# Performance work log

Measured on AMD Instinct MI355X. Metric: run time of the kernel, lower is better.

The kernel has to match this reference:

```python
import jax, jax.numpy as jnp
import numpy as np

IN_DIM = 1024
CTX_DIM = 768
NUM_HEADS = 16
HEAD_DIM = IN_DIM // NUM_HEADS
SCALE = 1.0 / float(np.sqrt(HEAD_DIM))


def setup_inputs() -> dict:
    key = jax.random.key(0)
    ks = jax.random.split(key, 10)
    B, NQ, NKV = 8, 1024, 512
    s_in = 1.0 / float(np.sqrt(IN_DIM))
    s_ctx = 1.0 / float(np.sqrt(CTX_DIM))
    return {
        "x": jax.random.normal(ks[0], (B, NQ, IN_DIM), dtype=jnp.float32),
        "context": jax.random.normal(ks[1], (B, NKV, CTX_DIM), dtype=jnp.float32),
        "Wq": jax.random.normal(ks[2], (IN_DIM, IN_DIM), dtype=jnp.float32) * s_in,
        "bq": jax.random.normal(ks[3], (IN_DIM,), dtype=jnp.float32) * 0.01,
        "Wk": jax.random.normal(ks[4], (IN_DIM, CTX_DIM), dtype=jnp.float32) * s_ctx,
        "bk": jax.random.normal(ks[5], (IN_DIM,), dtype=jnp.float32) * 0.01,
        "Wv": jax.random.normal(ks[6], (IN_DIM, CTX_DIM), dtype=jnp.float32) * s_ctx,
        "bv": jax.random.normal(ks[7], (IN_DIM,), dtype=jnp.float32) * 0.01,
        "Wo": jax.random.normal(ks[8], (IN_DIM, IN_DIM), dtype=jnp.float32) * s_in,
        "bo": jax.random.normal(ks[9], (IN_DIM,), dtype=jnp.float32) * 0.01,
    }


def reference(x, context, Wq, bq, Wk, bk, Wv, bv, Wo, bo):
    # Linear projections (torch Linear: y = x @ W.T + b)
    q = x @ Wq.T + bq              # [B, Nq, in_dim]
    k = context @ Wk.T + bk        # [B, Nkv, in_dim]
    v = context @ Wv.T + bv        # [B, Nkv, in_dim]
    B, NQ, _ = q.shape
    NKV = k.shape[1]
    q = q.reshape(B, NQ, NUM_HEADS, HEAD_DIM)
    k = k.reshape(B, NKV, NUM_HEADS, HEAD_DIM)
    v = v.reshape(B, NKV, NUM_HEADS, HEAD_DIM)
    attn = jnp.einsum('bihd,bjhd->bhij', q, k) * SCALE   # [B, H, Nq, Nkv]
    # the half-batch split in the original is mathematically identical to
    # a plain softmax over the last dim
    attn = jax.nn.softmax(attn, axis=-1)
    out = jnp.einsum('bhij,bjhd->bihd', attn, v)          # [B, Nq, H, Dh]
    out = out.reshape(B, NQ, IN_DIM)
    return out @ Wo.T + bo
```

## Files before the change

kernel.cpp:

```cpp
#include <hip/hip_runtime.h>
#include <math.h>

#define IN_DIM    1024
#define CTX_DIM   768
#define NUM_HEADS 16
#define HEAD_DIM  64
#define BATCH     8
#define NQ        1024
#define NKV       512
#define SCALE     0.125f

typedef __attribute__((ext_vector_type(8))) _Float16 f16x8;
typedef __attribute__((ext_vector_type(4))) _Float16 f16x4;
typedef __attribute__((ext_vector_type(4))) float    f32x4;

__device__ __forceinline__ void async16(const void* g, void* l) {
    __builtin_amdgcn_global_load_lds(
        (const __attribute__((address_space(1))) void*)g,
        (__attribute__((address_space(3))) void*)l, 16, 0, 0);
}

__global__ __launch_bounds__(256)
void cvt6(const float* __restrict__ s0, const float* __restrict__ s1,
          const float* __restrict__ s2, const float* __restrict__ s3,
          const float* __restrict__ s4, const float* __restrict__ s5,
          _Float16* __restrict__ dst)
{
    const int stride = gridDim.x * blockDim.x;
    for (int i = blockIdx.x * blockDim.x + threadIdx.x; i < 3801088; i += stride) {
        const float* s; int loc;
        if      (i < 2097152) { s = s0; loc = i; }
        else if (i < 2883584) { s = s1; loc = i - 2097152; }
        else if (i < 3145728) { s = s2; loc = i - 2883584; }
        else if (i < 3342336) { s = s3; loc = i - 3145728; }
        else if (i < 3538944) { s = s4; loc = i - 3342336; }
        else                  { s = s5; loc = i - 3538944; }
        float4 v = *(const float4*)(s + (size_t)loc * 4);
        f16x4 o;
        o.x = (_Float16)v.x; o.y = (_Float16)v.y;
        o.z = (_Float16)v.z; o.w = (_Float16)v.w;
        *(f16x4*)(dst + (size_t)i * 4) = o;
    }
}

template<int BN, typename OutT>
__global__ __launch_bounds__(256)
void gemm_h(const _Float16* __restrict__ A, const _Float16* __restrict__ W,
            const float* __restrict__ bias, OutT* __restrict__ C,
            int M, int N, int K)
{
    constexpr int BM = 128, BK = 64;
    constexpr int NF = BN / 32;
    __shared__ alignas(16) _Float16 As[BM * BK];
    __shared__ alignas(16) _Float16 Ws[BN * BK];

    const int tid = threadIdx.x;
    const int l   = tid & 63;
    const int w   = tid >> 6;
    const int wr  = w >> 1, wc = w & 1;
    const int m0  = blockIdx.y * BM;
    const int n0  = blockIdx.x * BN;

    f32x4 acc[4][NF];
    #pragma unroll
    for (int m = 0; m < 4; ++m)
        #pragma unroll
        for (int n = 0; n < NF; ++n)
            acc[m][n] = (f32x4){0.f, 0.f, 0.f, 0.f};

    const int nk = K / BK;
    for (int kt = 0; kt < nk; ++kt) {
        const int k0 = kt * BK;
        #pragma unroll
        for (int it = 0; it < 4; ++it) {
            int e = it * 256 + tid;
            int r = e >> 3, p = e & 7;
            async16(A + (size_t)(m0 + r) * K + k0 + ((p ^ (r & 7)) * 8),
                    &As[(size_t)(it * 256 + (tid & ~63)) * 8]);
        }
        #pragma unroll
        for (int it = 0; it < BN / 32; ++it) {
            int e = it * 256 + tid;
            int r = e >> 3, p = e & 7;
            async16(W + (size_t)(n0 + r) * K + k0 + ((p ^ (r & 7)) * 8),
                    &Ws[(size_t)(it * 256 + (tid & ~63)) * 8]);
        }
        __syncthreads();

        #pragma unroll
        for (int kk = 0; kk < 2; ++kk) {
            f16x8 af[4], bf[NF];
            #pragma unroll
            for (int m = 0; m < 4; ++m) {
                int rr = wr * 64 + m * 16 + (l & 15);
                int slot = (kk * 4 + (l >> 4)) ^ (rr & 7);
                af[m] = *(const f16x8*)&As[rr * 64 + slot * 8];
            }
            #pragma unroll
            for (int n = 0; n < NF; ++n) {
                int rr = wc * (BN / 2) + n * 16 + (l & 15);
                int slot = (kk * 4 + (l >> 4)) ^ (rr & 7);
                bf[n] = *(const f16x8*)&Ws[rr * 64 + slot * 8];
            }
            #pragma unroll
            for (int m = 0; m < 4; ++m)
                #pragma unroll
                for (int n = 0; n < NF; ++n)
                    acc[m][n] = __builtin_amdgcn_mfma_f32_16x16x32_f16(
                        af[m], bf[n], acc[m][n], 0, 0, 0);
        }
        __syncthreads();
    }

    float bv[NF];
    #pragma unroll
    for (int n = 0; n < NF; ++n)
        bv[n] = bias[n0 + wc * (BN / 2) + n * 16 + (l & 15)];
    #pragma unroll
    for (int m = 0; m < 4; ++m)
        #pragma unroll
        for (int n = 0; n < NF; ++n)
            #pragma unroll
            for (int r = 0; r < 4; ++r) {
                int row = m0 + wr * 64 + m * 16 + (l >> 4) * 4 + r;
                int col = n0 + wc * (BN / 2) + n * 16 + (l & 15);
                C[(size_t)row * N + col] = (OutT)(acc[m][n][r] + bv[n]);
            }
}

__global__ __launch_bounds__(256)
void transpose_v(const _Float16* __restrict__ Vh, _Float16* __restrict__ Vt)
{
    __shared__ alignas(16) _Float16 Ts[64 * 72];
    const int tid = threadIdx.x;
    const int kvt = blockIdx.x, h = blockIdx.y, b = blockIdx.z;
    const int kv0 = kvt * 64;
    #pragma unroll
    for (int it = 0; it < 2; ++it) {
        int g = it * 256 + tid;
        int kv = g >> 3, d0 = (g & 7) * 8;
        *(f16x8*)&Ts[kv * 72 + d0] =
            *(const f16x8*)(Vh + (size_t)(b * NKV + kv0 + kv) * IN_DIM + h * 64 + d0);
    }
    __syncthreads();
    #pragma unroll
    for (int it = 0; it < 2; ++it) {
        int g = it * 256 + tid;
        int d = g >> 3, k0 = (g & 7) * 8;
        f16x8 v;
        #pragma unroll
        for (int j = 0; j < 8; ++j) v[j] = Ts[(k0 + j) * 72 + d];
        *(f16x8*)(Vt + ((size_t)((b * 16 + h) * 64 + d)) * NKV + kv0 + k0) = v;
    }
}

__global__ __launch_bounds__(256)
void attn_mfma(const _Float16* __restrict__ Qh, const _Float16* __restrict__ Kh,
               const _Float16* __restrict__ Vt, _Float16* __restrict__ Ah)
{
    __shared__ alignas(16) _Float16 Ks[64 * 64];
    __shared__ alignas(16) _Float16 Vs[64 * 64];
    __shared__ alignas(16) _Float16 Pl[4][16 * 88];

    const int tid = threadIdx.x;
    const int l = tid & 63, w = tid >> 6;
    const int qt = blockIdx.x, h = blockIdx.y, b = blockIdx.z;
    const int q0 = qt * 64;

    f16x8 qa[2];
    {
        const _Float16* qp = Qh + (size_t)(b * NQ + q0 + w * 16 + (l & 15)) * IN_DIM
                                + h * 64 + (l >> 4) * 8;
        qa[0] = *(const f16x8*)qp;
        qa[1] = *(const f16x8*)(qp + 32);
    }

    float m_run[4], l_run[4];
    f32x4 of[4];
    #pragma unroll
    for (int r = 0; r < 4; ++r) { m_run[r] = -1e30f; l_run[r] = 0.f; }
    #pragma unroll
    for (int d = 0; d < 4; ++d) of[d] = (f32x4){0.f, 0.f, 0.f, 0.f};

    for (int kt = 0; kt < NKV / 64; ++kt) {
        const int kv0 = kt * 64;
        __syncthreads();
        #pragma unroll
        for (int it = 0; it < 2; ++it) {
            int e = it * 256 + tid;
            int r = e >> 3, p = e & 7;
            async16(Kh + (size_t)(b * NKV + kv0 + r) * IN_DIM + h * 64 + ((p ^ (r & 7)) * 8),
                    &Ks[(size_t)(it * 256 + (tid & ~63)) * 8]);
        }
        #pragma unroll
        for (int it = 0; it < 2; ++it) {
            int e = it * 256 + tid;
            int r = e >> 3, p = e & 7;
            async16(Vt + ((size_t)((b * 16 + h) * 64 + r)) * NKV + kv0 + ((p ^ (r & 7)) * 8),
                    &Vs[(size_t)(it * 256 + (tid & ~63)) * 8]);
        }
        __syncthreads();

        f32x4 sf[4];
        #pragma unroll
        for (int n = 0; n < 4; ++n) sf[n] = (f32x4){0.f, 0.f, 0.f, 0.f};
        #pragma unroll
        for (int kk = 0; kk < 2; ++kk)
            #pragma unroll
            for (int n = 0; n < 4; ++n) {
                int rr = n * 16 + (l & 15);
                int slot = (kk * 4 + (l >> 4)) ^ (rr & 7);
                f16x8 kb = *(const f16x8*)&Ks[rr * 64 + slot * 8];
                sf[n] = __builtin_amdgcn_mfma_f32_16x16x32_f16(qa[kk], kb, sf[n], 0, 0, 0);
            }

        float corr[4];
        #pragma unroll
        for (int r = 0; r < 4; ++r) {
            float mx = -1e30f;
            #pragma unroll
            for (int n = 0; n < 4; ++n) mx = fmaxf(mx, sf[n][r] * SCALE);
            #pragma unroll
            for (int off = 1; off < 16; off <<= 1) mx = fmaxf(mx, __shfl_xor(mx, off));
            float mnew = fmaxf(m_run[r], mx);
            corr[r] = __expf(m_run[r] - mnew);
            float rs = 0.f;
            #pragma unroll
            for (int n = 0; n < 4; ++n) {
                float p = __expf(sf[n][r] * SCALE - mnew);
                sf[n][r] = p;
                rs += p;
            }
            #pragma unroll
            for (int off = 1; off < 16; off <<= 1) rs += __shfl_xor(rs, off);
            l_run[r] = l_run[r] * corr[r] + rs;
            m_run[r] = mnew;
        }

        #pragma unroll
        for (int n = 0; n < 4; ++n)
            #pragma unroll
            for (int r = 0; r < 4; ++r)
                Pl[w][((l >> 4) * 4 + r) * 88 + n * 16 + (l & 15)] = (_Float16)sf[n][r];

        #pragma unroll
        for (int d = 0; d < 4; ++d)
            #pragma unroll
            for (int r = 0; r < 4; ++r) of[d][r] *= corr[r];

        #pragma unroll
        for (int kk = 0; kk < 2; ++kk) {
            f16x8 pa = *(const f16x8*)&Pl[w][(l & 15) * 88 + kk * 32 + (l >> 4) * 8];
            #pragma unroll
            for (int d = 0; d < 4; ++d) {
                int rr = d * 16 + (l & 15);
                int slot = (kk * 4 + (l >> 4)) ^ (rr & 7);
                f16x8 vb = *(const f16x8*)&Vs[rr * 64 + slot * 8];
                of[d] = __builtin_amdgcn_mfma_f32_16x16x32_f16(pa, vb, of[d], 0, 0, 0);
            }
        }
    }

    float inv[4];
    #pragma unroll
    for (int r = 0; r < 4; ++r) inv[r] = 1.f / l_run[r];
    #pragma unroll
    for (int d = 0; d < 4; ++d)
        #pragma unroll
        for (int r = 0; r < 4; ++r) {
            size_t row = (size_t)(b * NQ + q0 + w * 16 + (l >> 4) * 4 + r);
            Ah[row * IN_DIM + h * 64 + d * 16 + (l & 15)] = (_Float16)(of[d][r] * inv[r]);
        }
}

extern "C" void kernel_launch(void* const* d_in, const int* in_sizes, int n_in,
                              void* d_out, int out_size, void* d_ws, size_t ws_size,
                              hipStream_t stream)
{
    const float* x   = (const float*)d_in[0];
    const float* ctx = (const float*)d_in[1];
    const float* Wq  = (const float*)d_in[2];
    const float* bq  = (const float*)d_in[3];
    const float* Wk  = (const float*)d_in[4];
    const float* bk  = (const float*)d_in[5];
    const float* Wv  = (const float*)d_in[6];
    const float* bv  = (const float*)d_in[7];
    const float* Wo  = (const float*)d_in[8];
    const float* bo  = (const float*)d_in[9];
    float* out = (float*)d_out;

    _Float16* H = (_Float16*)d_ws;
    _Float16* xh   = H +        0;
    _Float16* ctxh = H +  8388608;
    _Float16* wqh  = H + 11534336;
    _Float16* wkh  = H + 12582912;
    _Float16* wvh  = H + 13369344;
    _Float16* woh  = H + 14155776;
    _Float16* Qh   = H + 15204352;
    _Float16* Kh   = H + 23592960;
    _Float16* Vh   = H + 27787264;
    _Float16* Vth  = H + 31981568;
    _Float16* Ah   = H + 36175872;

    const int MQ = BATCH * NQ;
    const int MK = BATCH * NKV;

    cvt6<<<2048, 256, 0, stream>>>(x, ctx, Wq, Wk, Wv, Wo, xh);

    gemm_h<128, _Float16><<<dim3(IN_DIM/128, MQ/128), 256, 0, stream>>>(
        xh, wqh, bq, Qh, MQ, IN_DIM, IN_DIM);
    gemm_h<64, _Float16><<<dim3(IN_DIM/64, MK/128), 256, 0, stream>>>(
        ctxh, wkh, bk, Kh, MK, IN_DIM, CTX_DIM);
    gemm_h<64, _Float16><<<dim3(IN_DIM/64, MK/128), 256, 0, stream>>>(
        ctxh, wvh, bv, Vh, MK, IN_DIM, CTX_DIM);

    transpose_v<<<dim3(NKV/64, NUM_HEADS, BATCH), 256, 0, stream>>>(Vh, Vth);

    attn_mfma<<<dim3(NQ/64, NUM_HEADS, BATCH), 256, 0, stream>>>(Qh, Kh, Vth, Ah);

    gemm_h<128, float><<<dim3(IN_DIM/128, MQ/128), 256, 0, stream>>>(
        Ah, woh, bo, out, MQ, IN_DIM, IN_DIM);
}
```

Before: 258.9 us.

## Double-buffer attention K/V, lazy softmax rescale, merge K/V GEMMs, swizzle tiles

The attention kernel now double-buffers its K/V tiles so the next tile loads while the current one computes. It also switches to exp2 with a pre-folded scale, skips the running-max rescale unless the max grows by more than 8, and raises wave priority around the MFMA sections. The GEMMs gain a block-index remap that interleaves tiles across XCDs, precomputed LDS offsets, and fp16 epilogues staged through LDS so the stores are vectorized. The K and V projections are merged into one launch. These changes target load latency, exp/rescale ALU work, scattered global stores and launch overhead, at the cost of more LDS and more complex code.

```diff
diff --git a/kernel.cpp b/kernel.cpp
--- a/kernel.cpp
+++ b/kernel.cpp
@@ -18,6 +18,10 @@
     __builtin_amdgcn_global_load_lds(
         (const __attribute__((address_space(1))) void*)g,
         (__attribute__((address_space(3))) void*)l, 16, 0, 0);
+}
+
+__device__ __forceinline__ float fexp2(float x) {
+    float r; asm("v_exp_f32 %0, %1" : "=v"(r) : "v"(x)); return r;
 }
 
 __global__ __launch_bounds__(256)
@@ -43,23 +47,51 @@
     }
 }
 
-template<int BN, typename OutT>
+template<int BN, int NN, typename OutT>
 __global__ __launch_bounds__(256)
-void gemm_h(const _Float16* __restrict__ A, const _Float16* __restrict__ W,
-            const float* __restrict__ bias, OutT* __restrict__ C,
+void gemm_h(const _Float16* __restrict__ A,
+            const _Float16* __restrict__ W0, const float* __restrict__ bias0, OutT* __restrict__ C0,
+            const _Float16* __restrict__ W1, const float* __restrict__ bias1, OutT* __restrict__ C1,
             int M, int N, int K)
 {
     constexpr int BM = 128, BK = 64;
     constexpr int NF = BN / 32;
-    __shared__ alignas(16) _Float16 As[BM * BK];
-    __shared__ alignas(16) _Float16 Ws[BN * BK];
+    constexpr int SZ_T = BM * BK + BN * BK;
+    constexpr int CL   = BN + 8;
+    constexpr int SZ_E = BM * CL;
+    constexpr int LDSZ = SZ_T > SZ_E ? SZ_T : SZ_E;
+    __shared__ alignas(16) _Float16 lds[LDSZ];
+    _Float16* As = lds;
+    _Float16* Ws = lds + BM * BK;
+
+    const _Float16* W   = blockIdx.y ? W1 : W0;
+    const float*   bias = blockIdx.y ? bias1 : bias0;
+    OutT*          C    = blockIdx.y ? C1 : C0;
 
     const int tid = threadIdx.x;
     const int l   = tid & 63;
     const int w   = tid >> 6;
     const int wr  = w >> 1, wc = w & 1;
-    const int m0  = blockIdx.y * BM;
-    const int n0  = blockIdx.x * BN;
+
+    const int per  = gridDim.x >> 3;
+    const int tile = (blockIdx.x & 7) * per + (blockIdx.x >> 3);
+    const int m0   = (tile / NN) * BM;
+    const int n0   = (tile % NN) * BN;
+
+    int aOff[2][4], bOff[2][NF];
+    #pragma unroll
+    for (int kk = 0; kk < 2; ++kk) {
+        #pragma unroll
+        for (int m = 0; m < 4; ++m) {
+            int rr = wr * 64 + m * 16 + (l & 15);
+            aOff[kk][m] = rr * 64 + (((kk * 4 + (l >> 4)) ^ (rr & 7)) * 8);
+        }
+        #pragma unroll
+        for (int n = 0; n < NF; ++n) {
+            int rr = wc * (BN / 2) + n * 16 + (l & 15);
+            bOff[kk][n] = rr * 64 + (((kk * 4 + (l >> 4)) ^ (rr & 7)) * 8);
+        }
+    }
 
     f32x4 acc[4][NF];
     #pragma unroll
@@ -91,17 +123,9 @@
         for (int kk = 0; kk < 2; ++kk) {
             f16x8 af[4], bf[NF];
             #pragma unroll
-            for (int m = 0; m < 4; ++m) {
-                int rr = wr * 64 + m * 16 + (l & 15);
-                int slot = (kk * 4 + (l >> 4)) ^ (rr & 7);
-                af[m] = *(const f16x8*)&As[rr * 64 + slot * 8];
-            }
-            #pragma unroll
-            for (int n = 0; n < NF; ++n) {
-                int rr = wc * (BN / 2) + n * 16 + (l & 15);
-                int slot = (kk * 4 + (l >> 4)) ^ (rr & 7);
-                bf[n] = *(const f16x8*)&Ws[rr * 64 + slot * 8];
-            }
+            for (int m = 0; m < 4; ++m) af[m] = *(const f16x8*)&As[aOff[kk][m]];
+            #pragma unroll
+            for (int n = 0; n < NF; ++n) bf[n] = *(const f16x8*)&Ws[bOff[kk][n]];
             #pragma unroll
             for (int m = 0; m < 4; ++m)
                 #pragma unroll
@@ -116,16 +140,38 @@
     #pragma unroll
     for (int n = 0; n < NF; ++n)
         bv[n] = bias[n0 + wc * (BN / 2) + n * 16 + (l & 15)];
-    #pragma unroll
-    for (int m = 0; m < 4; ++m)
-        #pragma unroll
-        for (int n = 0; n < NF; ++n)
-            #pragma unroll
-            for (int r = 0; r < 4; ++r) {
-                int row = m0 + wr * 64 + m * 16 + (l >> 4) * 4 + r;
-                int col = n0 + wc * (BN / 2) + n * 16 + (l & 15);
-                C[(size_t)row * N + col] = (OutT)(acc[m][n][r] + bv[n]);
-            }
+
+    if constexpr (sizeof(OutT) == 2) {
+        _Float16* Ce = lds;
+        #pragma unroll
+        for (int m = 0; m < 4; ++m)
+            #pragma unroll
+            for (int n = 0; n < NF; ++n)
+                #pragma unroll
+                for (int r = 0; r < 4; ++r) {
+                    int row = wr * 64 + m * 16 + (l >> 4) * 4 + r;
+                    int col = wc * (BN / 2) + n * 16 + (l & 15);
+                    Ce[row * CL + col] = (_Float16)(acc[m][n][r] + bv[n]);
+                }
+        __syncthreads();
+        constexpr int SPR = BN / 8;
+        for (int i = tid; i < BM * SPR; i += 256) {
+            int r = i / SPR, s = i % SPR;
+            *(f16x8*)((_Float16*)C + (size_t)(m0 + r) * N + n0 + s * 8) =
+                *(const f16x8*)&Ce[r * CL + s * 8];
+        }
+    } else {
+        #pragma unroll
+        for (int m = 0; m < 4; ++m)
+            #pragma unroll
+            for (int n = 0; n < NF; ++n)
+                #pragma unroll
+                for (int r = 0; r < 4; ++r) {
+                    int row = m0 + wr * 64 + m * 16 + (l >> 4) * 4 + r;
+                    int col = n0 + wc * (BN / 2) + n * 16 + (l & 15);
+                    C[(size_t)row * N + col] = (OutT)(acc[m][n][r] + bv[n]);
+                }
+    }
 }
 
 __global__ __launch_bounds__(256)
@@ -158,14 +204,44 @@
 void attn_mfma(const _Float16* __restrict__ Qh, const _Float16* __restrict__ Kh,
                const _Float16* __restrict__ Vt, _Float16* __restrict__ Ah)
 {
-    __shared__ alignas(16) _Float16 Ks[64 * 64];
-    __shared__ alignas(16) _Float16 Vs[64 * 64];
+    __shared__ alignas(16) _Float16 Ks[2][64 * 64];
+    __shared__ alignas(16) _Float16 Vs[2][64 * 64];
     __shared__ alignas(16) _Float16 Pl[4][16 * 88];
 
     const int tid = threadIdx.x;
     const int l = tid & 63, w = tid >> 6;
-    const int qt = blockIdx.x, h = blockIdx.y, b = blockIdx.z;
+    const int t  = (blockIdx.x & 7) * 256 + (blockIdx.x >> 3);
+    const int qt = t & 15, h = (t >> 4) & 15, b = t >> 8;
     const int q0 = qt * 64;
+
+    int frOff[2][4];
+    #pragma unroll
+    for (int kk = 0; kk < 2; ++kk)
+        #pragma unroll
+        for (int n = 0; n < 4; ++n) {
+            int rr = n * 16 + (l & 15);
+            frOff[kk][n] = rr * 64 + (((kk * 4 + (l >> 4)) ^ (rr & 7)) * 8);
+        }
+    const int pWr  = ((l >> 4) * 4) * 88 + (l & 15);
+    const int pRd0 = (l & 15) * 88 + (l >> 4) * 8;
+
+    const _Float16* Kbase = Kh + (size_t)(b * NKV) * IN_DIM + h * 64;
+    const _Float16* Vbase = Vt + ((size_t)((b * 16 + h) * 64)) * NKV;
+
+#define STAGE(buf, kv0) do {                                                   \
+        _Pragma("unroll")                                                      \
+        for (int it = 0; it < 2; ++it) {                                       \
+            int e = it * 256 + tid; int r = e >> 3, p = e & 7;                 \
+            async16(Kbase + (size_t)((kv0) + r) * IN_DIM + ((p ^ (r & 7)) * 8),\
+                    &Ks[buf][(it * 256 + (tid & ~63)) * 8]);                   \
+        }                                                                      \
+        _Pragma("unroll")                                                      \
+        for (int it = 0; it < 2; ++it) {                                       \
+            int e = it * 256 + tid; int r = e >> 3, p = e & 7;                 \
+            async16(Vbase + (size_t)r * NKV + (kv0) + ((p ^ (r & 7)) * 8),     \
+                    &Vs[buf][(it * 256 + (tid & ~63)) * 8]);                   \
+        }                                                                      \
+    } while (0)
 
     f16x8 qa[2];
     {
@@ -175,101 +251,98 @@
         qa[1] = *(const f16x8*)(qp + 32);
     }
 
-    float m_run[4], l_run[4];
+    float m2[4], lr[4];
     f32x4 of[4];
     #pragma unroll
-    for (int r = 0; r < 4; ++r) { m_run[r] = -1e30f; l_run[r] = 0.f; }
+    for (int r = 0; r < 4; ++r) { m2[r] = -1e30f; lr[r] = 0.f; }
     #pragma unroll
     for (int d = 0; d < 4; ++d) of[d] = (f32x4){0.f, 0.f, 0.f, 0.f};
 
+    STAGE(0, 0);
+    __syncthreads();
+
+    const float C2 = SCALE * 1.44269504f;
+
     for (int kt = 0; kt < NKV / 64; ++kt) {
-        const int kv0 = kt * 64;
+        const int cur = kt & 1;
+        if (kt < NKV / 64 - 1) STAGE(cur ^ 1, (kt + 1) * 64);
+
+        __builtin_amdgcn_s_setprio(1);
+        f32x4 sf[4];
+        #pragma unroll
+        for (int n = 0; n < 4; ++n) sf[n] = (f32x4){0.f, 0.f, 0.f, 0.f};
+        #pragma unroll
+        for (int kk = 0; kk < 2; ++kk)
+            #pragma unroll
+            for (int n = 0; n < 4; ++n)
+                sf[n] = __builtin_amdgcn_mfma_f32_16x16x32_f16(
+                    qa[kk], *(const f16x8*)&Ks[cur][frOff[kk][n]], sf[n], 0, 0, 0);
+        __builtin_amdgcn_s_setprio(0);
+
+        float t4[4][4], pmax[4];
+        bool need = false;
+        #pragma unroll
+        for (int r = 0; r < 4; ++r) {
+            float a0 = sf[0][r] * C2, a1 = sf[1][r] * C2;
+            float a2 = sf[2][r] * C2, a3 = sf[3][r] * C2;
+            t4[r][0] = a0; t4[r][1] = a1; t4[r][2] = a2; t4[r][3] = a3;
+            float mx = fmaxf(fmaxf(a0, a1), fmaxf(a2, a3));
+            #pragma unroll
+            for (int off = 1; off < 16; off <<= 1)
+                mx = fmaxf(mx, __shfl_xor(mx, off));
+            pmax[r] = mx;
+            need |= (mx > m2[r] + 8.f);
+        }
+        if (__any((int)need)) {
+            #pragma unroll
+            for (int r = 0; r < 4; ++r) {
+                float mn = fmaxf(m2[r], pmax[r]);
+                float corr = fexp2(m2[r] - mn);
+                m2[r] = mn;
+                lr[r] *= corr;
+                #pragma unroll
+                for (int d = 0; d < 4; ++d) of[d][r] *= corr;
+            }
+        }
+        #pragma unroll
+        for (int r = 0; r < 4; ++r) {
+            float p0 = fexp2(t4[r][0] - m2[r]);
+            float p1 = fexp2(t4[r][1] - m2[r]);
+            float p2 = fexp2(t4[r][2] - m2[r]);
+            float p3 = fexp2(t4[r][3] - m2[r]);
+            float rs = (p0 + p1) + (p2 + p3);
+            #pragma unroll
+            for (int off = 1; off < 16; off <<= 1)
+                rs += __shfl_xor(rs, off);
+            lr[r] += rs;
+            Pl[w][pWr + r * 88 +  0] = (_Float16)p0;
+            Pl[w][pWr + r * 88 + 16] = (_Float16)p1;
+            Pl[w][pWr + r * 88 + 32] = (_Float16)p2;
+            Pl[w][pWr + r * 88 + 48] = (_Float16)p3;
+        }
+
+        __builtin_amdgcn_s_setprio(1);
+        #pragma unroll
+        for (int kk = 0; kk < 2; ++kk) {
+            f16x8 pa = *(const f16x8*)&Pl[w][pRd0 + kk * 32];
+            #pragma unroll
+            for (int d = 0; d < 4; ++d)
+                of[d] = __builtin_amdgcn_mfma_f32_16x16x32_f16(
+                    pa, *(const f16x8*)&Vs[cur][frOff[kk][d]], of[d], 0, 0, 0);
+        }
+        __builtin_amdgcn_s_setprio(0);
         __syncthreads();
-        #pragma unroll
-        for (int it = 0; it < 2; ++it) {
-            int e = it * 256 + tid;
-            int r = e >> 3, p = e & 7;
-            async16(Kh + (size_t)(b * NKV + kv0 + r) * IN_DIM + h * 64 + ((p ^ (r & 7)) * 8),
-                    &Ks[(size_t)(it * 256 + (tid & ~63)) * 8]);
-        }
-        #pragma unroll
-        for (int it = 0; it < 2; ++it) {
-            int e = it * 256 + tid;
-            int r = e >> 3, p = e & 7;
-            async16(Vt + ((size_t)((b * 16 + h) * 64 + r)) * NKV + kv0 + ((p ^ (r & 7)) * 8),
-                    &Vs[(size_t)(it * 256 + (tid & ~63)) * 8]);
-        }
-        __syncthreads();
-
-        f32x4 sf[4];
-        #pragma unroll
-        for (int n = 0; n < 4; ++n) sf[n] = (f32x4){0.f, 0.f, 0.f, 0.f};
-        #pragma unroll
-        for (int kk = 0; kk < 2; ++kk)
-            #pragma unroll
-            for (int n = 0; n < 4; ++n) {
-                int rr = n * 16 + (l & 15);
-                int slot = (kk * 4 + (l >> 4)) ^ (rr & 7);
-                f16x8 kb = *(const f16x8*)&Ks[rr * 64 + slot * 8];
-                sf[n] = __builtin_amdgcn_mfma_f32_16x16x32_f16(qa[kk], kb, sf[n], 0, 0, 0);
-            }
-
-        float corr[4];
-        #pragma unroll
-        for (int r = 0; r < 4; ++r) {
-            float mx = -1e30f;
-            #pragma unroll
-            for (int n = 0; n < 4; ++n) mx = fmaxf(mx, sf[n][r] * SCALE);
-            #pragma unroll
-            for (int off = 1; off < 16; off <<= 1) mx = fmaxf(mx, __shfl_xor(mx, off));
-            float mnew = fmaxf(m_run[r], mx);
-            corr[r] = __expf(m_run[r] - mnew);
-            float rs = 0.f;
-            #pragma unroll
-            for (int n = 0; n < 4; ++n) {
-                float p = __expf(sf[n][r] * SCALE - mnew);
-                sf[n][r] = p;
-                rs += p;
-            }
-            #pragma unroll
-            for (int off = 1; off < 16; off <<= 1) rs += __shfl_xor(rs, off);
-            l_run[r] = l_run[r] * corr[r] + rs;
-            m_run[r] = mnew;
-        }
-
-        #pragma unroll
-        for (int n = 0; n < 4; ++n)
-            #pragma unroll
-            for (int r = 0; r < 4; ++r)
-                Pl[w][((l >> 4) * 4 + r) * 88 + n * 16 + (l & 15)] = (_Float16)sf[n][r];
-
-        #pragma unroll
-        for (int d = 0; d < 4; ++d)
-            #pragma unroll
-            for (int r = 0; r < 4; ++r) of[d][r] *= corr[r];
-
-        #pragma unroll
-        for (int kk = 0; kk < 2; ++kk) {
-            f16x8 pa = *(const f16x8*)&Pl[w][(l & 15) * 88 + kk * 32 + (l >> 4) * 8];
-            #pragma unroll
-            for (int d = 0; d < 4; ++d) {
-                int rr = d * 16 + (l & 15);
-                int slot = (kk * 4 + (l >> 4)) ^ (rr & 7);
-                f16x8 vb = *(const f16x8*)&Vs[rr * 64 + slot * 8];
-                of[d] = __builtin_amdgcn_mfma_f32_16x16x32_f16(pa, vb, of[d], 0, 0, 0);
-            }
-        }
-    }
-
-    float inv[4];
-    #pragma unroll
-    for (int r = 0; r < 4; ++r) inv[r] = 1.f / l_run[r];
+    }
+#undef STAGE
+
+    #pragma unroll
+    for (int r = 0; r < 4; ++r) lr[r] = 1.f / lr[r];
     #pragma unroll
     for (int d = 0; d < 4; ++d)
         #pragma unroll
         for (int r = 0; r < 4; ++r) {
             size_t row = (size_t)(b * NQ + q0 + w * 16 + (l >> 4) * 4 + r);
-            Ah[row * IN_DIM + h * 64 + d * 16 + (l & 15)] = (_Float16)(of[d][r] * inv[r]);
+            Ah[row * IN_DIM + h * 64 + d * 16 + (l & 15)] = (_Float16)(of[d][r] * lr[r]);
         }
 }
 
@@ -307,17 +380,15 @@
 
     cvt6<<<2048, 256, 0, stream>>>(x, ctx, Wq, Wk, Wv, Wo, xh);
 
-    gemm_h<128, _Float16><<<dim3(IN_DIM/128, MQ/128), 256, 0, stream>>>(
-        xh, wqh, bq, Qh, MQ, IN_DIM, IN_DIM);
-    gemm_h<64, _Float16><<<dim3(IN_DIM/64, MK/128), 256, 0, stream>>>(
-        ctxh, wkh, bk, Kh, MK, IN_DIM, CTX_DIM);
-    gemm_h<64, _Float16><<<dim3(IN_DIM/64, MK/128), 256, 0, stream>>>(
-        ctxh, wvh, bv, Vh, MK, IN_DIM, CTX_DIM);
+    gemm_h<128, 8, _Float16><<<dim3(512, 1), 256, 0, stream>>>(
+        xh, wqh, bq, Qh, wqh, bq, Qh, MQ, IN_DIM, IN_DIM);
+    gemm_h<64, 16, _Float16><<<dim3(512, 2), 256, 0, stream>>>(
+        ctxh, wkh, bk, Kh, wvh, bv, Vh, MK, IN_DIM, CTX_DIM);
 
     transpose_v<<<dim3(NKV/64, NUM_HEADS, BATCH), 256, 0, stream>>>(Vh, Vth);
 
-    attn_mfma<<<dim3(NQ/64, NUM_HEADS, BATCH), 256, 0, stream>>>(Qh, Kh, Vth, Ah);
-
-    gemm_h<128, float><<<dim3(IN_DIM/128, MQ/128), 256, 0, stream>>>(
-        Ah, woh, bo, out, MQ, IN_DIM, IN_DIM);
-}
+    attn_mfma<<<2048, 256, 0, stream>>>(Qh, Kh, Vth, Ah);
+
+    gemm_h<128, 8, float><<<dim3(512, 1), 256, 0, stream>>>(
+        Ah, woh, bo, out, woh, bo, out, MQ, IN_DIM, IN_DIM);
+}
```

New measurement: 252.7 us. -2.4%, faster.
